# Performance work log

Measured on AMD Instinct MI355X. Metric: run time of the kernel, lower is better.

The kernel has to match this reference:

```python
import jax, jax.numpy as jnp
import numpy as np

B, A, HR = 2, 180, 512
H_OUT = W_OUT = 512


def setup_inputs() -> dict:
    key = jax.random.key(0)
    k1, = jax.random.split(key, 1)
    sino = jax.random.normal(k1, (B, A, HR), dtype=jnp.float32)
    angles_deg = jnp.linspace(0.0, 180.0, A, endpoint=False, dtype=jnp.float32)
    return {"sino": sino, "angles_deg": angles_deg, "H": H_OUT, "W": W_OUT}


def _forward(sino, angles_deg, H, W):
    Bn, An, Hr = sino.shape
    pad = int(1.0 * 0.1 * min(H, W))  # pad_ratio = 1.0
    Hp, Wp = H + 2 * pad, W + 2 * pad

    # --- F.interpolate bilinear, align_corners=False: (A,B,Hr,1) -> (A,B,Hp,Wp).
    # Input width is 1, so width interp replicates the single column; only height interp matters.
    src = jnp.clip((jnp.arange(Hp, dtype=jnp.float32) + 0.5) * (Hr / Hp) - 0.5, 0.0, Hr - 1)
    i0 = jnp.floor(src).astype(jnp.int32)
    i1 = jnp.minimum(i0 + 1, Hr - 1)
    wH = src - i0.astype(jnp.float32)
    p = jnp.transpose(sino, (1, 0, 2)).astype(jnp.float32)  # (A,B,Hr)
    col = p[:, :, i0] * (1.0 - wH) + p[:, :, i1] * wH       # (A,B,Hp)
    proj = jnp.broadcast_to(col[:, :, :, None], (An, Bn, Hp, Wp))  # (A,B,Hp,Wp)

    # --- affine_grid (align_corners=False), sign = -1
    th = -jnp.deg2rad(angles_deg)
    c, s = jnp.cos(th), jnp.sin(th)                          # (A,)
    xs = (jnp.arange(Wp, dtype=jnp.float32) + 0.5) * (2.0 / Wp) - 1.0
    ys = (jnp.arange(Hp, dtype=jnp.float32) + 0.5) * (2.0 / Hp) - 1.0
    gx = c[:, None, None] * xs[None, None, :] - s[:, None, None] * ys[None, :, None]  # (A,Hp,Wp)
    gy = s[:, None, None] * xs[None, None, :] + c[:, None, None] * ys[None, :, None]

    # --- grid_sample bilinear, zeros padding, align_corners=False
    ix = ((gx + 1.0) * Wp - 1.0) * 0.5
    iy = ((gy + 1.0) * Hp - 1.0) * 0.5
    x0 = jnp.floor(ix).astype(jnp.int32); x1 = x0 + 1
    y0 = jnp.floor(iy).astype(jnp.int32); y1 = y0 + 1
    wx = ix - x0.astype(jnp.float32)
    wy = iy - y0.astype(jnp.float32)

    def corner(img, xi, yi, w):  # img (B,Hp,Wp); idx/w (Hp,Wp)
        valid = (xi >= 0) & (xi <= Wp - 1) & (yi >= 0) & (yi <= Hp - 1)
        xc = jnp.clip(xi, 0, Wp - 1)
        yc = jnp.clip(yi, 0, Hp - 1)
        return img[:, yc, xc] * (w * valid.astype(jnp.float32))[None]

    def sample(img, x0a, x1a, y0a, y1a, wxa, wya):
        return (corner(img, x0a, y0a, (1 - wxa) * (1 - wya)) +
                corner(img, x1a, y0a, wxa * (1 - wya)) +
                corner(img, x0a, y1a, (1 - wxa) * wya) +
                corner(img, x1a, y1a, wxa * wya))

    xr = jax.vmap(sample)(proj, x0, x1, y0, y1, wx, wy)      # (A,B,Hp,Wp)
    acc = xr.sum(axis=0) / (An + 1e-06)                      # (B,Hp,Wp)
    acc = acc[:, None, :, :]                                 # (B,1,Hp,Wp)
    if pad > 0:
        acc = acc[:, :, pad:Hp - pad, pad:Wp - pad]
    return acc


def reference(sino, angles_deg, H, W):
    return _forward(sino, angles_deg, H, W)
```

## Files before the change

kernel.cpp:

```cpp
#include <hip/hip_runtime.h>
#include <hip/hip_fp16.h>
#include <math.h>

#define B_N   2
#define A_N   180
#define HR_N  512
#define H_OUT 512
#define W_OUT 512
#define PAD   51
#define HP    614
#define WP    614
#define GUARD 80
#define HPP   (HP + 2*GUARD)
#define NPIX  (H_OUT * W_OUT)

#define TW    16
#define TH    8
#define QA    45
#define CH_Q  15
#define NCH   3
#define WIN   20


__device__ __forceinline__ float col_val(const float* __restrict__ sino,
                                         int b, int a, int yy) {
    if (yy < 0 || yy >= HP) return 0.0f;
    float src = ((float)yy + 0.5f) * ((float)HR_N / (float)HP) - 0.5f;
    src = fminf(fmaxf(src, 0.0f), (float)(HR_N - 1));
    int i0 = (int)floorf(src);
    int i1 = min(i0 + 1, HR_N - 1);
    float wH = src - (float)i0;
    const float* srow = sino + ((size_t)b * A_N + a) * HR_N;
    return srow[i0] * (1.0f - wH) + srow[i1] * wH;
}

__global__ void prep_kernel(const float* __restrict__ sino,
                            const float* __restrict__ angles,
                            uint2* __restrict__ pk2,
                            float2* __restrict__ tg) {
    int idx = blockIdx.x * blockDim.x + threadIdx.x;
    if (idx < A_N) {
        float th = -angles[idx] * (float)(M_PI / 180.0);
        tg[idx] = make_float2(cosf(th), sinf(th));
    }
    const int total = A_N * HPP;
    if (idx < total) {
        int y = idx % HPP;
        int a = idx / HPP;
        int yy = y - GUARD;
        float v00 = col_val(sino, 0, a, yy);
        float v10 = col_val(sino, 1, a, yy);
        float v01 = col_val(sino, 0, a, yy + 1);
        float v11 = col_val(sino, 1, a, yy + 1);
        __half2 lo = __floats2half2_rn(v00, v10);
        __half2 hi = __floats2half2_rn(v01, v11);
        uint2 u;
        u.x = *(unsigned int*)&lo;
        u.y = *(unsigned int*)&hi;
        pk2[idx] = u;
    }
}

template <bool INTERIOR>
__device__ __forceinline__ void bp_body(const uint2* __restrict__ pk2,
                                        const float4* __restrict__ s_cs,
                                        const unsigned* __restrict__ s_off,
                                        uint2* __restrict__ s_win,
                                        int t, int q, float X, float Y,
                                        float& a00, float& a01, float& a10, float& a11) {
    for (int ch = 0; ch < NCH; ++ch) {
        for (int e = t; e < 4 * CH_Q * WIN; e += 256) {
            int wid = e / WIN;
            int j   = e - wid * WIN;
            int qq  = wid / CH_Q;
            int la  = wid - qq * CH_Q;
            int a   = qq * QA + ch * CH_Q + la;
            s_win[e] = pk2[s_off[a] + (unsigned)j];
        }
        __syncthreads();

        const int abase = q * QA + ch * CH_Q;
        const int wbase = q * (CH_Q * WIN);
        if (INTERIOR) {
            __half2 h0 = __float2half2_rn(0.0f);
            __half2 h1 = __float2half2_rn(0.0f);
#pragma unroll
            for (int la = 0; la < CH_Q; ++la) {
                float4 cs = s_cs[abase + la];
                float c = cs.x, s = cs.y;
                float f0 = fmaf(s, X, fmaf(c, Y, cs.z));
                float f1 = f0 + s;
                int   li0 = (int)f0;  float wy0 = __builtin_amdgcn_fractf(f0);
                int   li1 = (int)f1;  float wy1 = f1 - (float)li1;
                uint2 cv0 = s_win[wbase + la * WIN + li0];
                uint2 cv1 = s_win[wbase + la * WIN + li1];
                __half2 lo0 = *(__half2*)&cv0.x, hi0 = *(__half2*)&cv0.y;
                __half2 lo1 = *(__half2*)&cv1.x, hi1 = *(__half2*)&cv1.y;
                h0 = __hadd2(h0, __hfma2(__float2half2_rn(wy0), __hsub2(hi0, lo0), lo0));
                h1 = __hadd2(h1, __hfma2(__float2half2_rn(wy1), __hsub2(hi1, lo1), lo1));
            }
            a00 += __low2float(h0);  a01 += __high2float(h0);
            a10 += __low2float(h1);  a11 += __high2float(h1);
        } else {
#pragma unroll
            for (int la = 0; la < CH_Q; ++la) {
                float4 cs = s_cs[abase + la];
                float c = cs.x, s = cs.y;
                float f0 = fmaf(s, X, fmaf(c, Y, cs.z));
                float f1 = f0 + s;
                int   li0 = (int)f0;  float wy0 = __builtin_amdgcn_fractf(f0);
                int   li1 = (int)f1;  float wy1 = f1 - (float)li1;
                uint2 cv0 = s_win[wbase + la * WIN + li0];
                uint2 cv1 = s_win[wbase + la * WIN + li1];
                __half2 lo0 = *(__half2*)&cv0.x, hi0 = *(__half2*)&cv0.y;
                __half2 lo1 = *(__half2*)&cv1.x, hi1 = *(__half2*)&cv1.y;
                __half2 r0 = __hfma2(__float2half2_rn(wy0), __hsub2(hi0, lo0), lo0);
                __half2 r1 = __hfma2(__float2half2_rn(wy1), __hsub2(hi1, lo1), lo1);
                float ix0 = fmaf(c, X, fmaf(-s, Y, 306.5f));
                float ix1 = ix0 + c;
                float xf0 = fminf(fmaxf(ix0 + 1.0f, 0.0f), 1.0f)
                          * fminf(fmaxf((float)WP - ix0, 0.0f), 1.0f);
                float xf1 = fminf(fmaxf(ix1 + 1.0f, 0.0f), 1.0f)
                          * fminf(fmaxf((float)WP - ix1, 0.0f), 1.0f);
                a00 = fmaf(xf0, __low2float(r0),  a00);
                a01 = fmaf(xf0, __high2float(r0), a01);
                a10 = fmaf(xf1, __low2float(r1),  a10);
                a11 = fmaf(xf1, __high2float(r1), a11);
            }
        }
        __syncthreads();
    }
}

__global__ __launch_bounds__(256, 4) void bp_kernel(const uint2* __restrict__ pk2,
                                                    const float2* __restrict__ tgv,
                                                    float* __restrict__ out) {
    __shared__ float4   s_cs[A_N];
    __shared__ unsigned s_off[A_N];
    __shared__ uint2    s_win[4 * CH_Q * WIN];
    __shared__ float    s_red[3][256];

    int t  = threadIdx.x;
    int tx = blockIdx.x, ty = blockIdx.y;
    float Xc = (float)(tx * TW) - 248.0f;
    float Yc = (float)(ty * TH) - 252.0f;

    if (t < A_N) {
        float2 cs = tgv[t];
        float iyc = fmaf(cs.y, Xc, fmaf(cs.x, Yc, 306.5f));
        int base = (int)floorf(iyc) - 9;
        s_cs[t]  = make_float4(cs.x, cs.y, 306.5f - (float)base, 0.0f);
        s_off[t] = (unsigned)(t * HPP + GUARD + base);
    }

    int q  = t >> 6;
    int tt = t & 63;
    int lx = (tt & 7) << 1;
    int ly = tt >> 3;
    float X = (float)(tx * TW + lx) - 255.5f;
    float Y = (float)(ty * TH + ly) - 255.5f;

    float a00 = 0.0f, a01 = 0.0f, a10 = 0.0f, a11 = 0.0f;
    __syncthreads();

    bool interior = (Xc * Xc + Yc * Yc) <= 87500.0f;
    if (interior)
        bp_body<true >(pk2, s_cs, s_off, s_win, t, q, X, Y, a00, a01, a10, a11);
    else
        bp_body<false>(pk2, s_cs, s_off, s_win, t, q, X, Y, a00, a01, a10, a11);

    int pix = ly * TW + lx;
    if (q != 0) {
        s_red[q - 1][pix]           = a00;
        s_red[q - 1][pix + 1]       = a10;
        s_red[q - 1][128 + pix]     = a01;
        s_red[q - 1][128 + pix + 1] = a11;
    }
    __syncthreads();
    if (q == 0) {
        const float inv = 1.0f / (180.0f + 1e-6f);
        float2 v0, v1;
        v0.x = (a00 + s_red[0][pix]       + s_red[1][pix]       + s_red[2][pix])       * inv;
        v0.y = (a10 + s_red[0][pix+1]     + s_red[1][pix+1]     + s_red[2][pix+1])     * inv;
        v1.x = (a01 + s_red[0][128+pix]   + s_red[1][128+pix]   + s_red[2][128+pix])   * inv;
        v1.y = (a11 + s_red[0][128+pix+1] + s_red[1][128+pix+1] + s_red[2][128+pix+1]) * inv;
        int idx = (ty * TH + ly) * W_OUT + (tx * TW + lx);
        *(float2*)(out + idx)        = v0;
        *(float2*)(out + NPIX + idx) = v1;
    }
}

extern "C" void kernel_launch(void* const* d_in, const int* in_sizes, int n_in,
                              void* d_out, int out_size, void* d_ws, size_t ws_size,
                              hipStream_t stream) {
    const float* sino   = (const float*)d_in[0];
    const float* angles = (const float*)d_in[1];
    char*   ws  = (char*)d_ws;
    uint2*  pk2 = (uint2*)ws;
    float2* tg  = (float2*)(ws + (size_t)A_N * HPP * sizeof(uint2));

    const int total = A_N * HPP;
    prep_kernel<<<(total + 255) / 256, 256, 0, stream>>>(sino, angles, pk2, tg);

    dim3 grid(W_OUT / TW, H_OUT / TH);
    bp_kernel<<<grid, 256, 0, stream>>>(pk2, tg, (float*)d_out);
}
```

Measured before the change: 83.51 us.

## Double output tile height so each thread computes two rows per angle

The tile grows from 16x8 to 16x16 pixels, so each thread now produces two pixel pairs eight rows apart. The staged projection window per angle widens from 20 to 24 entries to cover the taller tile. This halves the number of blocks and amortises the per-block window loads, sin/cos setup and barriers over twice the pixels. The cost is higher register pressure, a larger shared-memory window and reduction buffer, and half as many blocks to spread across the GPU. The offset array is also folded into the w field of the per-angle float4.

```diff
diff --git a/kernel.cpp b/kernel.cpp
--- a/kernel.cpp
+++ b/kernel.cpp
@@ -15,11 +15,12 @@
 #define NPIX  (H_OUT * W_OUT)
 
 #define TW    16
-#define TH    8
+#define TH    16
 #define QA    45
 #define CH_Q  15
 #define NCH   3
-#define WIN   20
+#define WIN   24
+#define CHUNK_E (4 * CH_Q * WIN)
 
 
 __device__ __forceinline__ float col_val(const float* __restrict__ sino,
@@ -61,71 +62,100 @@
     }
 }
 
+__device__ __forceinline__ __half2 interp(uint2 cv, float w) {
+    __half2 lo = *(__half2*)&cv.x, hi = *(__half2*)&cv.y;
+    return __hfma2(__float2half2_rn(w), __hsub2(hi, lo), lo);
+}
+
 template <bool INTERIOR>
 __device__ __forceinline__ void bp_body(const uint2* __restrict__ pk2,
                                         const float4* __restrict__ s_cs,
-                                        const unsigned* __restrict__ s_off,
                                         uint2* __restrict__ s_win,
                                         int t, int q, float X, float Y,
-                                        float& a00, float& a01, float& a10, float& a11) {
+                                        float& p00, float& p01, float& p10, float& p11,
+                                        float& q00, float& q01, float& q10, float& q11) {
     for (int ch = 0; ch < NCH; ++ch) {
-        for (int e = t; e < 4 * CH_Q * WIN; e += 256) {
+        for (int e = t; e < CHUNK_E; e += 256) {
             int wid = e / WIN;
             int j   = e - wid * WIN;
             int qq  = wid / CH_Q;
             int la  = wid - qq * CH_Q;
             int a   = qq * QA + ch * CH_Q + la;
-            s_win[e] = pk2[s_off[a] + (unsigned)j];
+            s_win[e] = pk2[__float_as_uint(s_cs[a].w) + (unsigned)j];
         }
         __syncthreads();
 
         const int abase = q * QA + ch * CH_Q;
         const int wbase = q * (CH_Q * WIN);
         if (INTERIOR) {
-            __half2 h0 = __float2half2_rn(0.0f);
-            __half2 h1 = __float2half2_rn(0.0f);
+            __half2 h00 = __float2half2_rn(0.0f);
+            __half2 h01 = __float2half2_rn(0.0f);
+            __half2 h10 = __float2half2_rn(0.0f);
+            __half2 h11 = __float2half2_rn(0.0f);
 #pragma unroll
             for (int la = 0; la < CH_Q; ++la) {
                 float4 cs = s_cs[abase + la];
                 float c = cs.x, s = cs.y;
-                float f0 = fmaf(s, X, fmaf(c, Y, cs.z));
-                float f1 = f0 + s;
-                int   li0 = (int)f0;  float wy0 = __builtin_amdgcn_fractf(f0);
-                int   li1 = (int)f1;  float wy1 = f1 - (float)li1;
-                uint2 cv0 = s_win[wbase + la * WIN + li0];
-                uint2 cv1 = s_win[wbase + la * WIN + li1];
-                __half2 lo0 = *(__half2*)&cv0.x, hi0 = *(__half2*)&cv0.y;
-                __half2 lo1 = *(__half2*)&cv1.x, hi1 = *(__half2*)&cv1.y;
-                h0 = __hadd2(h0, __hfma2(__float2half2_rn(wy0), __hsub2(hi0, lo0), lo0));
-                h1 = __hadd2(h1, __hfma2(__float2half2_rn(wy1), __hsub2(hi1, lo1), lo1));
+                float f00 = fmaf(s, X, fmaf(c, Y, cs.z));
+                float f01 = f00 + s;
+                float f10 = f00 + 8.0f * c;
+                float f11 = f10 + s;
+                int i00 = (int)f00;  float w00 = __builtin_amdgcn_fractf(f00);
+                int i01 = (int)f01;  float w01 = __builtin_amdgcn_fractf(f01);
+                int i10 = (int)f10;  float w10 = __builtin_amdgcn_fractf(f10);
+                int i11 = (int)f11;  float w11 = __builtin_amdgcn_fractf(f11);
+                const int wb = wbase + la * WIN;
+                uint2 v00 = s_win[wb + i00];
+                uint2 v01 = s_win[wb + i01];
+                uint2 v10 = s_win[wb + i10];
+                uint2 v11 = s_win[wb + i11];
+                h00 = __hadd2(h00, interp(v00, w00));
+                h01 = __hadd2(h01, interp(v01, w01));
+                h10 = __hadd2(h10, interp(v10, w10));
+                h11 = __hadd2(h11, interp(v11, w11));
             }
-            a00 += __low2float(h0);  a01 += __high2float(h0);
-            a10 += __low2float(h1);  a11 += __high2float(h1);
+            p00 += __low2float(h00);  p01 += __high2float(h00);
+            p10 += __low2float(h01);  p11 += __high2float(h01);
+            q00 += __low2float(h10);  q01 += __high2float(h10);
+            q10 += __low2float(h11);  q11 += __high2float(h11);
         } else {
 #pragma unroll
             for (int la = 0; la < CH_Q; ++la) {
                 float4 cs = s_cs[abase + la];
                 float c = cs.x, s = cs.y;
-                float f0 = fmaf(s, X, fmaf(c, Y, cs.z));
-                float f1 = f0 + s;
-                int   li0 = (int)f0;  float wy0 = __builtin_amdgcn_fractf(f0);
-                int   li1 = (int)f1;  float wy1 = f1 - (float)li1;
-                uint2 cv0 = s_win[wbase + la * WIN + li0];
-                uint2 cv1 = s_win[wbase + la * WIN + li1];
-                __half2 lo0 = *(__half2*)&cv0.x, hi0 = *(__half2*)&cv0.y;
-                __half2 lo1 = *(__half2*)&cv1.x, hi1 = *(__half2*)&cv1.y;
-                __half2 r0 = __hfma2(__float2half2_rn(wy0), __hsub2(hi0, lo0), lo0);
-                __half2 r1 = __hfma2(__float2half2_rn(wy1), __hsub2(hi1, lo1), lo1);
-                float ix0 = fmaf(c, X, fmaf(-s, Y, 306.5f));
-                float ix1 = ix0 + c;
-                float xf0 = fminf(fmaxf(ix0 + 1.0f, 0.0f), 1.0f)
-                          * fminf(fmaxf((float)WP - ix0, 0.0f), 1.0f);
-                float xf1 = fminf(fmaxf(ix1 + 1.0f, 0.0f), 1.0f)
-                          * fminf(fmaxf((float)WP - ix1, 0.0f), 1.0f);
-                a00 = fmaf(xf0, __low2float(r0),  a00);
-                a01 = fmaf(xf0, __high2float(r0), a01);
-                a10 = fmaf(xf1, __low2float(r1),  a10);
-                a11 = fmaf(xf1, __high2float(r1), a11);
+                float f00 = fmaf(s, X, fmaf(c, Y, cs.z));
+                float f01 = f00 + s;
+                float f10 = f00 + 8.0f * c;
+                float f11 = f10 + s;
+                int i00 = (int)f00;  float w00 = __builtin_amdgcn_fractf(f00);
+                int i01 = (int)f01;  float w01 = __builtin_amdgcn_fractf(f01);
+                int i10 = (int)f10;  float w10 = __builtin_amdgcn_fractf(f10);
+                int i11 = (int)f11;  float w11 = __builtin_amdgcn_fractf(f11);
+                const int wb = wbase + la * WIN;
+                __half2 r00 = interp(s_win[wb + i00], w00);
+                __half2 r01 = interp(s_win[wb + i01], w01);
+                __half2 r10 = interp(s_win[wb + i10], w10);
+                __half2 r11 = interp(s_win[wb + i11], w11);
+                float ix00 = fmaf(c, X, fmaf(-s, Y, 306.5f));
+                float ix01 = ix00 + c;
+                float ix10 = ix00 - 8.0f * s;
+                float ix11 = ix10 + c;
+                float xf00 = fminf(fmaxf(ix00 + 1.0f, 0.0f), 1.0f)
+                           * fminf(fmaxf((float)WP - ix00, 0.0f), 1.0f);
+                float xf01 = fminf(fmaxf(ix01 + 1.0f, 0.0f), 1.0f)
+                           * fminf(fmaxf((float)WP - ix01, 0.0f), 1.0f);
+                float xf10 = fminf(fmaxf(ix10 + 1.0f, 0.0f), 1.0f)
+                           * fminf(fmaxf((float)WP - ix10, 0.0f), 1.0f);
+                float xf11 = fminf(fmaxf(ix11 + 1.0f, 0.0f), 1.0f)
+                           * fminf(fmaxf((float)WP - ix11, 0.0f), 1.0f);
+                p00 = fmaf(xf00, __low2float(r00),  p00);
+                p01 = fmaf(xf00, __high2float(r00), p01);
+                p10 = fmaf(xf01, __low2float(r01),  p10);
+                p11 = fmaf(xf01, __high2float(r01), p11);
+                q00 = fmaf(xf10, __low2float(r10),  q00);
+                q01 = fmaf(xf10, __high2float(r10), q01);
+                q10 = fmaf(xf11, __low2float(r11),  q10);
+                q11 = fmaf(xf11, __high2float(r11), q11);
             }
         }
         __syncthreads();
@@ -135,22 +165,21 @@
 __global__ __launch_bounds__(256, 4) void bp_kernel(const uint2* __restrict__ pk2,
                                                     const float2* __restrict__ tgv,
                                                     float* __restrict__ out) {
-    __shared__ float4   s_cs[A_N];
-    __shared__ unsigned s_off[A_N];
-    __shared__ uint2    s_win[4 * CH_Q * WIN];
-    __shared__ float    s_red[3][256];
+    __shared__ float4 s_cs[A_N];
+    __shared__ uint2  s_win[CHUNK_E];
+    __shared__ float  s_red[3 * 64 * 9];
 
     int t  = threadIdx.x;
     int tx = blockIdx.x, ty = blockIdx.y;
     float Xc = (float)(tx * TW) - 248.0f;
-    float Yc = (float)(ty * TH) - 252.0f;
+    float Yc = (float)(ty * TH) - 248.0f;
 
     if (t < A_N) {
         float2 cs = tgv[t];
         float iyc = fmaf(cs.y, Xc, fmaf(cs.x, Yc, 306.5f));
-        int base = (int)floorf(iyc) - 9;
-        s_cs[t]  = make_float4(cs.x, cs.y, 306.5f - (float)base, 0.0f);
-        s_off[t] = (unsigned)(t * HPP + GUARD + base);
+        int base = (int)floorf(iyc) - 11;
+        s_cs[t] = make_float4(cs.x, cs.y, 306.5f - (float)base,
+                              __uint_as_float((unsigned)(t * HPP + GUARD + base)));
     }
 
     int q  = t >> 6;
@@ -160,33 +189,43 @@
     float X = (float)(tx * TW + lx) - 255.5f;
     float Y = (float)(ty * TH + ly) - 255.5f;
 
-    float a00 = 0.0f, a01 = 0.0f, a10 = 0.0f, a11 = 0.0f;
+    float p00 = 0.0f, p01 = 0.0f, p10 = 0.0f, p11 = 0.0f;
+    float q00 = 0.0f, q01 = 0.0f, q10 = 0.0f, q11 = 0.0f;
     __syncthreads();
 
     bool interior = (Xc * Xc + Yc * Yc) <= 87500.0f;
     if (interior)
-        bp_body<true >(pk2, s_cs, s_off, s_win, t, q, X, Y, a00, a01, a10, a11);
+        bp_body<true >(pk2, s_cs, s_win, t, q, X, Y, p00, p01, p10, p11, q00, q01, q10, q11);
     else
-        bp_body<false>(pk2, s_cs, s_off, s_win, t, q, X, Y, a00, a01, a10, a11);
-
-    int pix = ly * TW + lx;
+        bp_body<false>(pk2, s_cs, s_win, t, q, X, Y, p00, p01, p10, p11, q00, q01, q10, q11);
+
     if (q != 0) {
-        s_red[q - 1][pix]           = a00;
-        s_red[q - 1][pix + 1]       = a10;
-        s_red[q - 1][128 + pix]     = a01;
-        s_red[q - 1][128 + pix + 1] = a11;
+        float* r = &s_red[((q - 1) * 64 + tt) * 9];
+        r[0] = p00; r[1] = p01; r[2] = p10; r[3] = p11;
+        r[4] = q00; r[5] = q01; r[6] = q10; r[7] = q11;
     }
     __syncthreads();
     if (q == 0) {
         const float inv = 1.0f / (180.0f + 1e-6f);
-        float2 v0, v1;
-        v0.x = (a00 + s_red[0][pix]       + s_red[1][pix]       + s_red[2][pix])       * inv;
-        v0.y = (a10 + s_red[0][pix+1]     + s_red[1][pix+1]     + s_red[2][pix+1])     * inv;
-        v1.x = (a01 + s_red[0][128+pix]   + s_red[1][128+pix]   + s_red[2][128+pix])   * inv;
-        v1.y = (a11 + s_red[0][128+pix+1] + s_red[1][128+pix+1] + s_red[2][128+pix+1]) * inv;
-        int idx = (ty * TH + ly) * W_OUT + (tx * TW + lx);
-        *(float2*)(out + idx)        = v0;
-        *(float2*)(out + NPIX + idx) = v1;
+        const float* r0 = &s_red[tt * 9];
+        const float* r1 = &s_red[(64 + tt) * 9];
+        const float* r2 = &s_red[(128 + tt) * 9];
+        int col  = tx * TW + lx;
+        int idx0 = (ty * TH + ly) * W_OUT + col;
+        int idx1 = idx0 + 8 * W_OUT;
+        float2 o;
+        o.x = (p00 + r0[0] + r1[0] + r2[0]) * inv;
+        o.y = (p10 + r0[2] + r1[2] + r2[2]) * inv;
+        *(float2*)(out + idx0) = o;
+        o.x = (p01 + r0[1] + r1[1] + r2[1]) * inv;
+        o.y = (p11 + r0[3] + r1[3] + r2[3]) * inv;
+        *(float2*)(out + NPIX + idx0) = o;
+        o.x = (q00 + r0[4] + r1[4] + r2[4]) * inv;
+        o.y = (q10 + r0[6] + r1[6] + r2[6]) * inv;
+        *(float2*)(out + idx1) = o;
+        o.x = (q01 + r0[5] + r1[5] + r2[5]) * inv;
+        o.y = (q11 + r0[7] + r1[7] + r2[7]) * inv;
+        *(float2*)(out + NPIX + idx1) = o;
     }
 }
 
```

Result: no change. 82.42 us, median of 2 (-1.3%).
